# Performance work log

Hardware: AMD Instinct MI355X
Metric: run time of the kernel (lower is better)

## Reference

```python
import jax, jax.numpy as jnp
import numpy as np

DIM = 1024
H_MID = max(8, DIM // 2)   # 512
H_LOW = max(8, DIM // 4)   # 256


def setup_inputs() -> dict:
    key = jax.random.key(0)
    ks = jax.random.split(key, 10)
    s = lambda fan_in: 1.0 / np.sqrt(fan_in)
    x = jax.random.normal(ks[0], (4, 8192, DIM), dtype=jnp.float32)
    return {
        "x": x,
        "gamma": jnp.ones((DIM,), jnp.float32),
        "beta": jnp.zeros((DIM,), jnp.float32),
        "W1": jax.random.uniform(ks[1], (DIM, H_MID), jnp.float32, -s(DIM), s(DIM)),
        "b1": jax.random.uniform(ks[2], (H_MID,), jnp.float32, -s(DIM), s(DIM)),
        "W2": jax.random.uniform(ks[3], (H_MID, H_MID), jnp.float32, -s(H_MID), s(H_MID)),
        "b2": jax.random.uniform(ks[4], (H_MID,), jnp.float32, -s(H_MID), s(H_MID)),
        "W3": jax.random.uniform(ks[5], (H_MID, H_LOW), jnp.float32, -s(H_MID), s(H_MID)),
        "b3": jax.random.uniform(ks[6], (H_LOW,), jnp.float32, -s(H_MID), s(H_MID)),
        "W4": jax.random.uniform(ks[7], (H_LOW, DIM), jnp.float32, -s(H_LOW), s(H_LOW)),
        "b4": jax.random.uniform(ks[8], (DIM,), jnp.float32, -s(H_LOW), s(H_LOW)),
    }


def _layernorm(x, gamma, beta, eps=1e-5):
    mu = jnp.mean(x, axis=-1, keepdims=True)
    var = jnp.mean(jnp.square(x - mu), axis=-1, keepdims=True)
    return (x - mu) * jax.lax.rsqrt(var + eps) * gamma + beta


def reference(x, gamma, beta, W1, b1, W2, b2, W3, b3, W4, b4):
    gelu = lambda h: jax.nn.gelu(h, approximate=False)  # torch default: exact erf GELU
    h = _layernorm(x, gamma, beta)                      # (B,S,D)
    h = gelu(jnp.einsum("bsd,dm->bsm", h, W1) + b1)    # (B,S,D/2)
    h = gelu(jnp.einsum("bsm,mn->bsn", h, W2) + b2)    # (B,S,D/2)
    h = gelu(jnp.einsum("bsn,nl->bsl", h, W3) + b3)    # (B,S,D/4)
    h = jnp.einsum("bsl,ld->bsd", h, W4) + b4          # (B,S,D)
    return x + h
```

## Files before the change

### kernel.cpp

```cpp
#include <hip/hip_runtime.h>


typedef short short8 __attribute__((ext_vector_type(8)));
typedef float floatx4 __attribute__((ext_vector_type(4)));
typedef unsigned short ushort4v __attribute__((ext_vector_type(4)));

__device__ __forceinline__ unsigned short f2bf(float f) {
    union { float f; unsigned int u; } a; a.f = f;
    unsigned int u = a.u;
    return (unsigned short)((u + 0x7FFFu + ((u >> 16) & 1u)) >> 16);
}

__device__ __forceinline__ float gelu_exact(float v) {
    return 0.5f * v * (1.0f + erff(v * 0.70710678118654752f));
}

__device__ __forceinline__ void gl_lds16(const unsigned short* g, unsigned short* l) {
    __builtin_amdgcn_global_load_lds(
        (const __attribute__((address_space(1))) void*)g,
        (__attribute__((address_space(3))) void*)l, 16, 0, 0);
}

__global__ __launch_bounds__(256) void conv_w_kernel(
    const float* __restrict__ W, const float* __restrict__ scale,
    unsigned short* __restrict__ Wt, int K, int N) {
    int t = blockIdx.x * 256 + threadIdx.x;
    if (t >= K * N) return;
    int k = t / N, n = t - k * N;
    float v = W[t];
    if (scale) v *= scale[k];
    Wt[(size_t)n * K + k] = f2bf(v);
}

__global__ __launch_bounds__(256) void u1c1_init_kernel(
    const float* __restrict__ b1, float* __restrict__ u1, float* __restrict__ c1,
    int N) {
    int n = blockIdx.x * 256 + threadIdx.x;
    if (n >= N) return;
    u1[n] = 0.f;
    c1[n] = b1[n];
}

__global__ __launch_bounds__(256) void u1c1_kernel(
    const float* __restrict__ W1, const float* __restrict__ gamma,
    const float* __restrict__ beta, float* __restrict__ u1,
    float* __restrict__ c1) {
    const int N = 512;
    __shared__ float gs[16], bs[16];
    int n = threadIdx.x;
    int k0 = blockIdx.x * 16;
    if (n < 16) { gs[n] = gamma[k0 + n]; bs[n] = beta[k0 + n]; }
    __syncthreads();
    float ua = 0.f, ca = 0.f, ub = 0.f, cb = 0.f;
#pragma unroll
    for (int i = 0; i < 16; i++) {
        float w0 = W1[(size_t)(k0 + i) * N + n];
        float w1 = W1[(size_t)(k0 + i) * N + n + 256];
        ua += gs[i] * w0; ca += bs[i] * w0;
        ub += gs[i] * w1; cb += bs[i] * w1;
    }
    atomicAdd(&u1[n], ua);       atomicAdd(&c1[n], ca);
    atomicAdd(&u1[n + 256], ub); atomicAdd(&c1[n + 256], cb);
}

__global__ __launch_bounds__(256) void ln_stats_kernel(
    const float* __restrict__ x, float* __restrict__ mu, float* __restrict__ rs,
    unsigned short* __restrict__ xb) {
    const int D = 1024;
    int row = blockIdx.x * 4 + (threadIdx.x >> 6);
    int lane = threadIdx.x & 63;
    const float4* xr = (const float4*)(x + (size_t)row * D);
    float s = 0.f, ss = 0.f;
#pragma unroll
    for (int i = 0; i < 4; i++) {
        float4 v = xr[lane + 64 * i];
        s  += v.x + v.y + v.z + v.w;
        ss += v.x * v.x + v.y * v.y + v.z * v.z + v.w * v.w;
        if (xb) {
            ushort4v o;
            o.x = f2bf(v.x); o.y = f2bf(v.y); o.z = f2bf(v.z); o.w = f2bf(v.w);
            *(ushort4v*)(xb + (size_t)row * D + 4 * (lane + 64 * i)) = o;
        }
    }
#pragma unroll
    for (int off = 32; off; off >>= 1) {
        s  += __shfl_xor(s, off);
        ss += __shfl_xor(ss, off);
    }
    if (lane == 0) {
        float m = s * (1.0f / 1024.0f);
        mu[row] = m;
        rs[row] = rsqrtf(ss * (1.0f / 1024.0f) - m * m + 1e-5f);
    }
}

template <int EPMODE, bool AF32>
__global__ __launch_bounds__(256) void gemm_kernel(
    const void* __restrict__ Aptr, const unsigned short* __restrict__ Bt,
    void* __restrict__ Out, int N, int K,
    const float* __restrict__ bias,
    const float* __restrict__ u1,
    const float* __restrict__ mu,
    const float* __restrict__ rs,
    const float* __restrict__ resid)
{
    constexpr int BM = 128, BN = 128, BK = 32;
    __shared__ unsigned short As[BM][BK];
    __shared__ unsigned short Bs[BN][BK];

    const int tid  = threadIdx.x;
    const int wave = tid >> 6;
    const int lane = tid & 63;
    const int q    = lane >> 4;
    const int l16  = lane & 15;
    const int wm   = wave & 1;
    const int wn   = wave >> 1;
    const int m0   = blockIdx.y * BM;
    const int n0   = blockIdx.x * BN;

    const int sr = tid >> 2;
    const int sc = tid & 3;
    unsigned short* lA = &As[0][0] + ((tid >> 6) << 9);
    unsigned short* lB = &Bs[0][0] + ((tid >> 6) << 9);
    const unsigned short* gb0 = Bt + (size_t)(n0 + sr) * K + sc * 8;
    const unsigned short* ga0 = nullptr;
    if (!AF32) ga0 = (const unsigned short*)Aptr + (size_t)(m0 + sr) * K + sc * 8;

    floatx4 acc[4][4] = {};

    for (int k0 = 0; k0 < K; k0 += BK) {
        if (AF32) {
            const float* A = (const float*)Aptr;
            int c = tid & 7, r0 = tid >> 3;
#pragma unroll
            for (int i = 0; i < 4; i++) {
                int r = r0 + 32 * i;
                float4 v = *(const float4*)(A + (size_t)(m0 + r) * K + k0 + c * 4);
                unsigned short* dst = &As[r][c * 4];
                dst[0] = f2bf(v.x); dst[1] = f2bf(v.y);
                dst[2] = f2bf(v.z); dst[3] = f2bf(v.w);
            }
        } else {
            gl_lds16(ga0 + k0, lA);
            gl_lds16(ga0 + k0 + (size_t)64 * K, lA + 2048);
        }
        gl_lds16(gb0 + k0, lB);
        gl_lds16(gb0 + k0 + (size_t)64 * K, lB + 2048);
        __syncthreads();

        short8 a[4], b[4];
#pragma unroll
        for (int mt = 0; mt < 4; mt++)
            a[mt] = *(const short8*)&As[wm * 64 + mt * 16 + l16][q * 8];
#pragma unroll
        for (int nt = 0; nt < 4; nt++)
            b[nt] = *(const short8*)&Bs[wn * 64 + nt * 16 + l16][q * 8];
#pragma unroll
        for (int mt = 0; mt < 4; mt++)
#pragma unroll
            for (int nt = 0; nt < 4; nt++)
                acc[mt][nt] = __builtin_amdgcn_mfma_f32_16x16x32_bf16(
                    a[mt], b[nt], acc[mt][nt], 0, 0, 0);
        __syncthreads();
    }

#pragma unroll
    for (int mt = 0; mt < 4; mt++) {
#pragma unroll
        for (int r = 0; r < 4; r++) {
            int row = m0 + wm * 64 + mt * 16 + q * 4 + r;
            float rsv = 0.f, muv = 0.f;
            if (EPMODE == 0) { rsv = rs[row]; muv = mu[row]; }
#pragma unroll
            for (int nt = 0; nt < 4; nt++) {
                int col = n0 + wn * 64 + nt * 16 + l16;
                float v = acc[mt][nt][r];
                if constexpr (EPMODE == 0) {
                    v = rsv * (v - muv * u1[col]) + bias[col];
                    v = gelu_exact(v);
                    ((unsigned short*)Out)[(size_t)row * N + col] = f2bf(v);
                } else if constexpr (EPMODE == 1) {
                    v = gelu_exact(v + bias[col]);
                    ((unsigned short*)Out)[(size_t)row * N + col] = f2bf(v);
                } else {
                    v = v + bias[col] + resid[(size_t)row * N + col];
                    ((float*)Out)[(size_t)row * N + col] = v;
                }
            }
        }
    }
}

extern "C" void kernel_launch(void* const* d_in, const int* in_sizes, int n_in,
                              void* d_out, int out_size, void* d_ws, size_t ws_size,
                              hipStream_t stream) {
    const float* x     = (const float*)d_in[0];
    const float* gamma = (const float*)d_in[1];
    const float* beta  = (const float*)d_in[2];
    const float* W1    = (const float*)d_in[3];
    const float* b1    = (const float*)d_in[4];
    const float* W2    = (const float*)d_in[5];
    const float* b2    = (const float*)d_in[6];
    const float* W3    = (const float*)d_in[7];
    const float* b3    = (const float*)d_in[8];
    const float* W4    = (const float*)d_in[9];
    const float* b4    = (const float*)d_in[10];
    float* out = (float*)d_out;

    const int D = 1024, H1 = 512, H2 = 512, H3 = 256;
    const int M = in_sizes[0] / D;

    char* ws = (char*)d_ws;
    unsigned short* Wt1 = (unsigned short*)(ws + 0);
    unsigned short* Wt2 = (unsigned short*)(ws + 1048576);
    unsigned short* Wt3 = (unsigned short*)(ws + 1572864);
    unsigned short* Wt4 = (unsigned short*)(ws + 1835008);
    float* u1           = (float*)(ws + 2359296);
    float* c1           = (float*)(ws + 2361344);
    float* muv          = (float*)(ws + 2363392);
    float* rsv          = (float*)(ws + 2494464);
    unsigned short* h1  = (unsigned short*)(ws + 2625536);
    unsigned short* h2  = (unsigned short*)(ws + 36179968);
    unsigned short* h3  = h1;
    size_t base_end     = 36179968 + (size_t)M * H2 * 2;
    unsigned short* xb  = (unsigned short*)(ws + base_end);
    bool use_xb = (ws_size >= base_end + (size_t)M * D * 2);

    conv_w_kernel<<<(D * H1 + 255) / 256, 256, 0, stream>>>(W1, gamma, Wt1, D,  H1);
    conv_w_kernel<<<(H1 * H2 + 255) / 256, 256, 0, stream>>>(W2, nullptr, Wt2, H1, H2);
    conv_w_kernel<<<(H2 * H3 + 255) / 256, 256, 0, stream>>>(W3, nullptr, Wt3, H2, H3);
    conv_w_kernel<<<(H3 * D + 255) / 256, 256, 0, stream>>>(W4, nullptr, Wt4, H3, D);
    u1c1_init_kernel<<<(H1 + 255) / 256, 256, 0, stream>>>(b1, u1, c1, H1);
    u1c1_kernel<<<D / 16, 256, 0, stream>>>(W1, gamma, beta, u1, c1);

    ln_stats_kernel<<<M / 4, 256, 0, stream>>>(x, muv, rsv, use_xb ? xb : nullptr);

    if (use_xb) {
        gemm_kernel<0, false><<<dim3(H1 / 128, M / 128), 256, 0, stream>>>(
            xb, Wt1, h1,  H1, D,  c1, u1, muv, rsv, nullptr);
    } else {
        gemm_kernel<0, true ><<<dim3(H1 / 128, M / 128), 256, 0, stream>>>(
            x,  Wt1, h1,  H1, D,  c1, u1, muv, rsv, nullptr);
    }
    gemm_kernel<1, false><<<dim3(H2 / 128, M / 128), 256, 0, stream>>>(
        h1, Wt2, h2,  H2, H1, b2, nullptr, nullptr, nullptr, nullptr);
    gemm_kernel<1, false><<<dim3(H3 / 128, M / 128), 256, 0, stream>>>(
        h2, Wt3, h3,  H3, H2, b3, nullptr, nullptr, nullptr, nullptr);
    gemm_kernel<2, false><<<dim3(D  / 128, M / 128), 256, 0, stream>>>(
        h3, Wt4, out, D,  H3, b4, nullptr, nullptr, nullptr, x);
}
```

Measured before the change: 471.3 us.

## Use tanh-approx GELU, bf16 residual, XCD-aware block mapping, and fused weight conversion

Replaces the exact erf GELU with a tanh approximation built from hardware exp2 and rcp, to cut epilogue transcendental cost. The final GEMM now reads the residual from the bf16 copy of x instead of fp32, halving that read traffic. Blocks are remapped so that row tiles spread across the XCDs, the four weight-conversion launches are merged into one, and the epilogue hoists the per-column bias and u1 loads. The tanh GELU and bf16 residual lose accuracy against the exact fp32 reference, and may exceed the tolerance.

```diff
diff --git a/kernel.cpp b/kernel.cpp
--- a/kernel.cpp
+++ b/kernel.cpp
@@ -11,8 +11,16 @@
     return (unsigned short)((u + 0x7FFFu + ((u >> 16) & 1u)) >> 16);
 }
 
-__device__ __forceinline__ float gelu_exact(float v) {
-    return 0.5f * v * (1.0f + erff(v * 0.70710678118654752f));
+__device__ __forceinline__ float bf2f(unsigned short h) {
+    union { unsigned int u; float f; } a; a.u = ((unsigned int)h) << 16;
+    return a.f;
+}
+
+__device__ __forceinline__ float gelu_fast(float v) {
+    float u = 0.7978845608f * v * (1.0f + 0.044715f * v * v);
+    float e = __builtin_amdgcn_exp2f(u * 2.885390082f);
+    float t = 1.0f - 2.0f * __builtin_amdgcn_rcpf(1.0f + e);
+    return 0.5f * v * (1.0f + t);
 }
 
 __device__ __forceinline__ void gl_lds16(const unsigned short* g, unsigned short* l) {
@@ -21,14 +29,23 @@
         (__attribute__((address_space(3))) void*)l, 16, 0, 0);
 }
 
-__global__ __launch_bounds__(256) void conv_w_kernel(
-    const float* __restrict__ W, const float* __restrict__ scale,
-    unsigned short* __restrict__ Wt, int K, int N) {
-    int t = blockIdx.x * 256 + threadIdx.x;
-    if (t >= K * N) return;
-    int k = t / N, n = t - k * N;
+__global__ __launch_bounds__(256) void conv_all_kernel(
+    const float* __restrict__ W1, const float* __restrict__ W2,
+    const float* __restrict__ W3, const float* __restrict__ W4,
+    const float* __restrict__ gamma,
+    unsigned short* __restrict__ Wt1, unsigned short* __restrict__ Wt2,
+    unsigned short* __restrict__ Wt3, unsigned short* __restrict__ Wt4) {
+    int b = blockIdx.x;
+    const float* W; unsigned short* Wt; int K, N; const float* sc = nullptr;
+    if (b < 2048)      { W = W1; Wt = Wt1; K = 1024; N = 512;  sc = gamma; }
+    else if (b < 3072) { W = W2; Wt = Wt2; K = 512;  N = 512;  b -= 2048; }
+    else if (b < 3584) { W = W3; Wt = Wt3; K = 512;  N = 256;  b -= 3072; }
+    else               { W = W4; Wt = Wt4; K = 256;  N = 1024; b -= 3584; }
+    int t = b * 256 + threadIdx.x;
+    int sh = 31 - __clz(N);
+    int k = t >> sh, n = t & (N - 1);
     float v = W[t];
-    if (scale) v *= scale[k];
+    if (sc) v *= sc[k];
     Wt[(size_t)n * K + k] = f2bf(v);
 }
 
@@ -94,7 +111,7 @@
     }
 }
 
-template <int EPMODE, bool AF32>
+template <int EPMODE, bool AF32, int NBN>
 __global__ __launch_bounds__(256) void gemm_kernel(
     const void* __restrict__ Aptr, const unsigned short* __restrict__ Bt,
     void* __restrict__ Out, int N, int K,
@@ -102,7 +119,7 @@
     const float* __restrict__ u1,
     const float* __restrict__ mu,
     const float* __restrict__ rs,
-    const float* __restrict__ resid)
+    const void* __restrict__ resid)
 {
     constexpr int BM = 128, BN = 128, BK = 32;
     __shared__ unsigned short As[BM][BK];
@@ -115,13 +132,17 @@
     const int l16  = lane & 15;
     const int wm   = wave & 1;
     const int wn   = wave >> 1;
-    const int m0   = blockIdx.y * BM;
-    const int n0   = blockIdx.x * BN;
+
+    const int id   = blockIdx.x;
+    const int xcd  = id & 7;
+    const int slot = id >> 3;
+    const int m0   = (xcd + 8 * (slot / NBN)) * BM;
+    const int n0   = (slot % NBN) * BN;
 
     const int sr = tid >> 2;
     const int sc = tid & 3;
-    unsigned short* lA = &As[0][0] + ((tid >> 6) << 9);
-    unsigned short* lB = &Bs[0][0] + ((tid >> 6) << 9);
+    unsigned short* lA = &As[0][0] + (wave << 9);
+    unsigned short* lB = &Bs[0][0] + (wave << 9);
     const unsigned short* gb0 = Bt + (size_t)(n0 + sr) * K + sc * 8;
     const unsigned short* ga0 = nullptr;
     if (!AF32) ga0 = (const unsigned short*)Aptr + (size_t)(m0 + sr) * K + sc * 8;
@@ -165,25 +186,28 @@
     }
 
 #pragma unroll
-    for (int mt = 0; mt < 4; mt++) {
-#pragma unroll
-        for (int r = 0; r < 4; r++) {
-            int row = m0 + wm * 64 + mt * 16 + q * 4 + r;
-            float rsv = 0.f, muv = 0.f;
-            if (EPMODE == 0) { rsv = rs[row]; muv = mu[row]; }
-#pragma unroll
-            for (int nt = 0; nt < 4; nt++) {
-                int col = n0 + wn * 64 + nt * 16 + l16;
+    for (int nt = 0; nt < 4; nt++) {
+        const int col = n0 + wn * 64 + nt * 16 + l16;
+        const float bv = bias[col];
+        const float uv = (EPMODE == 0) ? u1[col] : 0.f;
+#pragma unroll
+        for (int mt = 0; mt < 4; mt++) {
+#pragma unroll
+            for (int r = 0; r < 4; r++) {
+                const int row = m0 + wm * 64 + mt * 16 + q * 4 + r;
                 float v = acc[mt][nt][r];
                 if constexpr (EPMODE == 0) {
-                    v = rsv * (v - muv * u1[col]) + bias[col];
-                    v = gelu_exact(v);
+                    v = rs[row] * (v - mu[row] * uv) + bv;
+                    v = gelu_fast(v);
                     ((unsigned short*)Out)[(size_t)row * N + col] = f2bf(v);
                 } else if constexpr (EPMODE == 1) {
-                    v = gelu_exact(v + bias[col]);
+                    v = gelu_fast(v + bv);
                     ((unsigned short*)Out)[(size_t)row * N + col] = f2bf(v);
+                } else if constexpr (EPMODE == 2) {
+                    v = v + bv + ((const float*)resid)[(size_t)row * N + col];
+                    ((float*)Out)[(size_t)row * N + col] = v;
                 } else {
-                    v = v + bias[col] + resid[(size_t)row * N + col];
+                    v = v + bv + bf2f(((const unsigned short*)resid)[(size_t)row * N + col]);
                     ((float*)Out)[(size_t)row * N + col] = v;
                 }
             }
@@ -226,26 +250,31 @@
     unsigned short* xb  = (unsigned short*)(ws + base_end);
     bool use_xb = (ws_size >= base_end + (size_t)M * D * 2);
 
-    conv_w_kernel<<<(D * H1 + 255) / 256, 256, 0, stream>>>(W1, gamma, Wt1, D,  H1);
-    conv_w_kernel<<<(H1 * H2 + 255) / 256, 256, 0, stream>>>(W2, nullptr, Wt2, H1, H2);
-    conv_w_kernel<<<(H2 * H3 + 255) / 256, 256, 0, stream>>>(W3, nullptr, Wt3, H2, H3);
-    conv_w_kernel<<<(H3 * D + 255) / 256, 256, 0, stream>>>(W4, nullptr, Wt4, H3, D);
+    const int NBM = M / 128;
+
+    conv_all_kernel<<<4608, 256, 0, stream>>>(W1, W2, W3, W4, gamma,
+                                              Wt1, Wt2, Wt3, Wt4);
     u1c1_init_kernel<<<(H1 + 255) / 256, 256, 0, stream>>>(b1, u1, c1, H1);
     u1c1_kernel<<<D / 16, 256, 0, stream>>>(W1, gamma, beta, u1, c1);
 
     ln_stats_kernel<<<M / 4, 256, 0, stream>>>(x, muv, rsv, use_xb ? xb : nullptr);
 
     if (use_xb) {
-        gemm_kernel<0, false><<<dim3(H1 / 128, M / 128), 256, 0, stream>>>(
+        gemm_kernel<0, false, 4><<<4 * NBM, 256, 0, stream>>>(
             xb, Wt1, h1,  H1, D,  c1, u1, muv, rsv, nullptr);
     } else {
-        gemm_kernel<0, true ><<<dim3(H1 / 128, M / 128), 256, 0, stream>>>(
+        gemm_kernel<0, true, 4><<<4 * NBM, 256, 0, stream>>>(
             x,  Wt1, h1,  H1, D,  c1, u1, muv, rsv, nullptr);
     }
-    gemm_kernel<1, false><<<dim3(H2 / 128, M / 128), 256, 0, stream>>>(
+    gemm_kernel<1, false, 4><<<4 * NBM, 256, 0, stream>>>(
         h1, Wt2, h2,  H2, H1, b2, nullptr, nullptr, nullptr, nullptr);
-    gemm_kernel<1, false><<<dim3(H3 / 128, M / 128), 256, 0, stream>>>(
+    gemm_kernel<1, false, 2><<<2 * NBM, 256, 0, stream>>>(
         h2, Wt3, h3,  H3, H2, b3, nullptr, nullptr, nullptr, nullptr);
-    gemm_kernel<2, false><<<dim3(D  / 128, M / 128), 256, 0, stream>>>(
-        h3, Wt4, out, D,  H3, b4, nullptr, nullptr, nullptr, x);
-}
+    if (use_xb) {
+        gemm_kernel<3, false, 8><<<8 * NBM, 256, 0, stream>>>(
+            h3, Wt4, out, D,  H3, b4, nullptr, nullptr, nullptr, xb);
+    } else {
+        gemm_kernel<2, false, 8><<<8 * NBM, 256, 0, stream>>>(
+            h3, Wt4, out, D,  H3, b4, nullptr, nullptr, nullptr, x);
+    }
+}
```

New measurement: 426.2 us. 1.11x faster.
